# Performance work log

Hardware: AMD Instinct MI355X
Metric: run time of the kernel (lower is better)

## Reference

```python
import jax, jax.numpy as jnp
import numpy as np

B, S, H = 4, 1024, 1024
NH, HD = 16, 64  # num heads, head dim


def setup_inputs() -> dict:
    key = jax.random.key(0)
    ks = jax.random.split(key, 7)
    scale = 1.0 / np.sqrt(H)
    return {
        "hidden_states": jax.random.normal(ks[0], (B, S, H), jnp.float32),
        "attention_mask": jnp.zeros((B, 1, 1, S), jnp.float32),
        "Wq": jax.random.normal(ks[1], (H, H), jnp.float32) * scale,
        "bq": jnp.zeros((H,), jnp.float32),
        "Wk": jax.random.normal(ks[2], (H, H), jnp.float32) * scale,
        "bk": jnp.zeros((H,), jnp.float32),
        "Wv": jax.random.normal(ks[3], (H, H), jnp.float32) * scale,
        "bv": jnp.zeros((H,), jnp.float32),
    }


def _heads(x):
    # [B,S,H] -> [B,NH,S,HD]
    return x.reshape(x.shape[0], x.shape[1], NH, HD).transpose(0, 2, 1, 3)


def reference(hidden_states, attention_mask, Wq, bq, Wk, bk, Wv, bv):
    q = _heads(hidden_states @ Wq + bq)  # [B,NH,S,HD]
    k = _heads(hidden_states @ Wk + bk)
    v = _heads(hidden_states @ Wv + bv)
    scores = jnp.einsum("bhqd,bhkd->bhqk", q, k) / np.sqrt(HD)
    scores = scores + attention_mask  # broadcast additive mask
    probs = jax.nn.softmax(scores, axis=-1)  # dropout p=0 (eval)
    ctx = jnp.einsum("bhqk,bhkd->bhqd", probs, v)
    # [B,NH,S,HD] -> [B,S,H]
    return ctx.transpose(0, 2, 1, 3).reshape(hidden_states.shape[0], hidden_states.shape[1], NH * HD)
```

## Files before the change

kernel.cpp:

```cpp
#include <hip/hip_runtime.h>
#include <hip/hip_bf16.h>

typedef __bf16 bf16_t;
typedef __bf16 bf16x8 __attribute__((ext_vector_type(8)));
typedef float f32x4 __attribute__((ext_vector_type(4)));
typedef float f32x8 __attribute__((ext_vector_type(8)));
typedef float f32x16 __attribute__((ext_vector_type(16)));
typedef unsigned uint2v __attribute__((ext_vector_type(2)));

#define MFMA16(a, b, c) __builtin_amdgcn_mfma_f32_16x16x32_bf16((a), (b), (c), 0, 0, 0)
#define MFMA32(a, b, c) __builtin_amdgcn_mfma_f32_32x32x16_bf16((a), (b), (c), 0, 0, 0)

static constexpr int BB = 4, SS = 1024, HH = 1024, NHEAD = 16, HDIM = 64;
static constexpr int MM = BB * SS;

__device__ __forceinline__ void gload_lds16(const void* g, void* l) {
  __builtin_amdgcn_global_load_lds((const __attribute__((address_space(1))) void*)g,
                                   (__attribute__((address_space(3))) void*)l, 16, 0, 0);
}

#if __has_builtin(__builtin_amdgcn_permlane32_swap)
#define PSWAP(a, b)                                                    \
  {                                                                    \
    uint2v _r = __builtin_amdgcn_permlane32_swap((a), (b), false, false); \
    (a) = _r.x;                                                        \
    (b) = _r.y;                                                        \
  }
#else
#define PSWAP(a, b) asm("v_permlane32_swap_b32 %0, %1" : "+v"(a), "+v"(b))
#endif

__device__ __forceinline__ float EXP2(float x) {
  float r;
  asm("v_exp_f32 %0, %1" : "=v"(r) : "v"(x));
  return r;
}

__global__ __launch_bounds__(256) void prep_kernel(const float* __restrict__ hs,
                                                   const float* __restrict__ Wq,
                                                   const float* __restrict__ Wk,
                                                   const float* __restrict__ Wv,
                                                   bf16_t* __restrict__ hiddenB,
                                                   bf16_t* __restrict__ WT) {
  const int t = threadIdx.x;
  if (blockIdx.x < 2048) {
    int i = (blockIdx.x * 256 + t) * 8;
    float4 a = *(const float4*)(hs + i);
    float4 b = *(const float4*)(hs + i + 4);
    union { int4 i4; bf16_t h[8]; } u;
    u.h[0] = (bf16_t)a.x; u.h[1] = (bf16_t)a.y; u.h[2] = (bf16_t)a.z; u.h[3] = (bf16_t)a.w;
    u.h[4] = (bf16_t)b.x; u.h[5] = (bf16_t)b.y; u.h[6] = (bf16_t)b.z; u.h[7] = (bf16_t)b.w;
    *(int4*)(hiddenB + i) = u.i4;
  } else {
    __shared__ float tile[32][33];
    int id = blockIdx.x - 2048;
    int z = id >> 10;
    int rem = id & 1023;
    int bx = rem & 31, by = rem >> 5;
    const float* W = (z == 0) ? Wq : (z == 1) ? Wk : Wv;
    bf16_t* Out = WT + (size_t)z * HH * HH;
    int tx = t & 31, ty = t >> 5;
    int x0 = bx * 32;
    int y0 = by * 32;
    for (int j = ty; j < 32; j += 8)
      tile[j][tx] = W[(size_t)(y0 + j) * HH + x0 + tx];
    __syncthreads();
    for (int j = ty; j < 32; j += 8)
      Out[(size_t)(x0 + j) * HH + y0 + tx] = (bf16_t)tile[tx][j];
  }
}

#define BMT 128
#define BNT 384
#define BKT 64
#define NTL 16
#define BUFBYTES 65536

__global__ __launch_bounds__(512, 2) void qkv_gemm2(const bf16_t* __restrict__ hiddenB,
                                                    const bf16_t* __restrict__ WT,
                                                    const float* __restrict__ bq,
                                                    const float* __restrict__ bk,
                                                    const float* __restrict__ bv,
                                                    bf16_t* __restrict__ Qo,
                                                    bf16_t* __restrict__ Ko,
                                                    bf16_t* __restrict__ Vt) {
  __shared__ bf16_t smem[2 * BUFBYTES / 2];

  const int wg = blockIdx.x;
  const int id = (wg & 7) * 32 + (wg >> 3);
  const int nb = id & 7;
  const int mb = id >> 3;

  const int t = threadIdx.x;
  const int lane = t & 63;
  const int w = t >> 6;
  const int wr = w >> 2;
  const int wc = w & 3;
  const int lr = lane & 15;
  const int g4 = lane >> 4;

  const unsigned schunk = (((unsigned)(t & 7)) ^ ((unsigned)((t >> 3) & 7))) << 4;
  const char* Ag = (const char*)hiddenB + (size_t)(mb * BMT) * 2048;
  const char* Bg = (const char*)WT + (size_t)(nb * BNT) * 2048;

  auto stage = [&](const char* gb, int growbase, int kbyte, char* ldsdest) {
    gload_lds16(gb + (size_t)(growbase + (t >> 3)) * 2048 + kbyte + schunk,
                ldsdest + w * 1024);
  };
  const unsigned axor = ((unsigned)(lr & 7)) << 4;

  f32x4 acc[4][6] = {};

  {
    char* S0 = (char*)smem;
    stage(Ag, 0, 0, S0);
    stage(Ag, 64, 0, S0 + 8192);
#pragma unroll
    for (int i = 0; i < 6; ++i) stage(Bg, i * 64, 0, S0 + 16384 + i * 8192);
  }
  asm volatile("s_waitcnt vmcnt(0)" ::: "memory");
  __builtin_amdgcn_s_barrier();

  for (int j = 0; j < NTL; ++j) {
    const char* Ab = (const char*)smem + (j & 1) * BUFBYTES;
    const char* Bb = Ab + 16384;
    char* Sb = (char*)smem + ((j + 1) & 1) * BUFBYTES;
    const int kb = (j + 1) * 128;
    const bool st = (j + 1 < NTL);

    if (st) { stage(Ag, 0, kb, Sb); stage(Ag, 64, kb, Sb + 8192); }

    bf16x8 af[4][2];
#pragma unroll
    for (int mi = 0; mi < 4; ++mi)
#pragma unroll
      for (int ks = 0; ks < 2; ++ks)
        af[mi][ks] = *(const bf16x8*)(Ab + (size_t)(wr * 64 + mi * 16 + lr) * 128 +
                                      (((unsigned)(ks * 64 + g4 * 16)) ^ axor));

#pragma unroll
    for (int p = 0; p < 3; ++p) {
      if (st) {
        stage(Bg, (2 * p) * 64, kb, Sb + 16384 + (2 * p) * 8192);
        stage(Bg, (2 * p + 1) * 64, kb, Sb + 16384 + (2 * p + 1) * 8192);
      }
      bf16x8 b0[2], b1[2];
#pragma unroll
      for (int ks = 0; ks < 2; ++ks) {
        b0[ks] = *(const bf16x8*)(Bb + (size_t)(wc * 96 + (2 * p) * 16 + lr) * 128 +
                                  (((unsigned)(ks * 64 + g4 * 16)) ^ axor));
        b1[ks] = *(const bf16x8*)(Bb + (size_t)(wc * 96 + (2 * p + 1) * 16 + lr) * 128 +
                                  (((unsigned)(ks * 64 + g4 * 16)) ^ axor));
      }
      __builtin_amdgcn_s_setprio(1);
#pragma unroll
      for (int mi = 0; mi < 4; ++mi)
#pragma unroll
        for (int ks = 0; ks < 2; ++ks) {
          acc[mi][2 * p] = MFMA16(af[mi][ks], b0[ks], acc[mi][2 * p]);
          acc[mi][2 * p + 1] = MFMA16(af[mi][ks], b1[ks], acc[mi][2 * p + 1]);
        }
      __builtin_amdgcn_s_setprio(0);
    }

    if (st) {
      asm volatile("s_waitcnt vmcnt(0)" ::: "memory");
      __builtin_amdgcn_s_barrier();
    }
  }

#pragma unroll
  for (int ni = 0; ni < 6; ++ni) {
    int col = nb * BNT + wc * 96 + ni * 16 + lr;
    int z = col >> 10;
    int ci = col & 1023;
    const float* bias = (z == 0) ? bq : (z == 1) ? bk : bv;
    float bia = bias[ci];
    int hh = ci >> 6, d = ci & 63;
    if (z < 2) {
      bf16_t* Out = (z == 0) ? Qo : Ko;
#pragma unroll
      for (int mi = 0; mi < 4; ++mi) {
#pragma unroll
        for (int r = 0; r < 4; ++r) {
          int row = mb * BMT + wr * 64 + mi * 16 + g4 * 4 + r;
          int b = row >> 10, s = row & 1023;
          Out[((size_t)(b * NHEAD + hh) * SS + s) * HDIM + d] = (bf16_t)(acc[mi][ni][r] + bia);
        }
      }
    } else {
#pragma unroll
      for (int mi = 0; mi < 4; ++mi) {
        int row0 = mb * BMT + wr * 64 + mi * 16 + g4 * 4;
        int b = row0 >> 10, s0 = row0 & 1023;
        float v0 = acc[mi][ni][0] + bia, v1 = acc[mi][ni][1] + bia;
        float v2 = acc[mi][ni][2] + bia, v3 = acc[mi][ni][3] + bia;
        unsigned u0, u1;
        asm("v_cvt_pk_bf16_f32 %0, %1, %2" : "=v"(u0) : "v"(v0), "v"(v1));
        asm("v_cvt_pk_bf16_f32 %0, %1, %2" : "=v"(u1) : "v"(v2), "v"(v3));
        uint2 pv; pv.x = u0; pv.y = u1;
        *(uint2*)&Vt[((size_t)(b * NHEAD + hh) * HDIM + d) * SS + s0] = pv;
      }
    }
  }
}

__global__ __launch_bounds__(512, 4) void attn8_kernel(const bf16_t* __restrict__ Q,
                                                       const bf16_t* __restrict__ K,
                                                       const bf16_t* __restrict__ Vt,
                                                       const float* __restrict__ mask,
                                                       float* __restrict__ out) {
  __shared__ bf16_t KVsm[2][2][2][64 * 64];
  __shared__ float Msm[SS];

  const int wg = blockIdx.x;
  const int id = (wg & 7) * 64 + (wg >> 3);
  const int xblk = id & 7;
  const int bh = id >> 3;

  const int b = bh >> 4;
  const int h = bh & 15;
  const int t = threadIdx.x;
  const int lane = t & 63;
  const int w = t >> 6;
  const int wl = w & 3;
  const int half = w >> 2;
  const int l31 = lane & 31;
  const int hi = lane >> 5;
  const int q0 = xblk * 128 + wl * 32;
  const int kvbase = half * 512;

  const bf16_t* Qh = Q + (size_t)bh * SS * HDIM;
  const bf16_t* Kh = K + (size_t)bh * SS * HDIM;
  const bf16_t* Vh = Vt + (size_t)bh * HDIM * SS;

  const float L2E = 1.4426950408889634f;
  if (t < 256) {
    float4 mv = *(const float4*)&mask[(size_t)b * SS + t * 4];
    mv.x = mv.x * L2E - 16.f; mv.y = mv.y * L2E - 16.f;
    mv.z = mv.z * L2E - 16.f; mv.w = mv.w * L2E - 16.f;
    *(float4*)&Msm[t * 4] = mv;
  }

  bf16x8 qb[4];
#pragma unroll
  for (int c = 0; c < 4; ++c) {
    bf16x8 q = *(const bf16x8*)&Qh[(size_t)(q0 + l31) * HDIM + c * 16 + hi * 8];
#pragma unroll
    for (int e = 0; e < 8; ++e) q[e] = (bf16_t)((float)q[e] * (0.125f * L2E));
    qb[c] = q;
  }

  const int srow = lane >> 3;
  const unsigned gcol = ((lane & 7) * 16) ^ (srow << 4);
  const unsigned swz = (unsigned)((l31 & 7) << 4);

  auto stageKV = [&](int tile, int buf) {
    const int kv0 = kvbase + tile * 64;
#pragma unroll
    for (int i = 0; i < 2; ++i) {
      int rbase = wl * 16 + i * 8;
      gload_lds16((const char*)Kh + (size_t)(kv0 + rbase + srow) * 128 + gcol,
                  (char*)&KVsm[half][buf][0][0] + (size_t)rbase * 128);
      gload_lds16((const char*)Vh + (size_t)(rbase + srow) * 2048 + (size_t)kv0 * 2 + gcol,
                  (char*)&KVsm[half][buf][1][0] + (size_t)rbase * 128);
    }
  };

  f32x16 acc0 = {}, acc1 = {};
  f32x8 la = {}, lb = {};

  stageKV(0, 0);
  asm volatile("s_waitcnt vmcnt(0) lgkmcnt(0)" ::: "memory");
  __builtin_amdgcn_s_barrier();

  for (int tt = 0; tt < 8; ++tt) {
    if (tt + 1 < 8) stageKV(tt + 1, (tt + 1) & 1);
    const char* Kb = (const char*)&KVsm[half][tt & 1][0][0];
    const char* Vb = (const char*)&KVsm[half][tt & 1][1][0];
    const int kv0 = kvbase + tt * 64;

    f32x16 st0 = {}, st1 = {};
    __builtin_amdgcn_s_setprio(1);
#pragma unroll
    for (int c = 0; c < 4; ++c) {
      bf16x8 kf0 = *(const bf16x8*)(Kb + (size_t)l31 * 128 + ((unsigned)(c * 32 + hi * 16) ^ swz));
      st0 = MFMA32(kf0, qb[c], st0);
    }
#pragma unroll
    for (int c = 0; c < 4; ++c) {
      bf16x8 kf1 = *(const bf16x8*)(Kb + (size_t)(32 + l31) * 128 + ((unsigned)(c * 32 + hi * 16) ^ swz));
      st1 = MFMA32(kf1, qb[c], st1);
    }
    __builtin_amdgcn_s_setprio(0);

#pragma unroll
    for (int k2 = 0; k2 < 8; ++k2) {
      int off = 8 * (k2 >> 1) + 4 * hi + 2 * (k2 & 1);
      float2 m0v = *(const float2*)&Msm[kv0 + off];
      float2 m1v = *(const float2*)&Msm[kv0 + 32 + off];
      st0[2 * k2] += m0v.x; st0[2 * k2 + 1] += m0v.y;
      st1[2 * k2] += m1v.x; st1[2 * k2 + 1] += m1v.y;
    }
#pragma unroll
    for (int r = 0; r < 16; ++r) st0[r] = EXP2(st0[r]);
#pragma unroll
    for (int r = 0; r < 16; ++r) st1[r] = EXP2(st1[r]);

#pragma unroll
    for (int r = 0; r < 8; ++r) {
      la[r] += st0[r] + st0[r + 8];
      lb[r] += st1[r] + st1[r + 8];
    }

    unsigned wd0[8], wd1[8];
#pragma unroll
    for (int k2 = 0; k2 < 8; ++k2) {
      unsigned r0, r1;
      float a0f = st0[2 * k2], a1f = st0[2 * k2 + 1];
      float b0f = st1[2 * k2], b1f = st1[2 * k2 + 1];
      asm("v_cvt_pk_bf16_f32 %0, %1, %2" : "=v"(r0) : "v"(a0f), "v"(a1f));
      asm("v_cvt_pk_bf16_f32 %0, %1, %2" : "=v"(r1) : "v"(b0f), "v"(b1f));
      wd0[k2] = r0; wd1[k2] = r1;
    }
    unsigned a0 = wd0[0], b0 = wd0[2]; PSWAP(a0, b0);
    unsigned a1 = wd0[1], b1 = wd0[3]; PSWAP(a1, b1);
    unsigned a2 = wd0[4], b2 = wd0[6]; PSWAP(a2, b2);
    unsigned a3 = wd0[5], b3 = wd0[7]; PSWAP(a3, b3);
    unsigned c0 = wd1[0], d0 = wd1[2]; PSWAP(c0, d0);
    unsigned c1 = wd1[1], d1 = wd1[3]; PSWAP(c1, d1);
    unsigned c2 = wd1[4], d2 = wd1[6]; PSWAP(c2, d2);
    unsigned c3 = wd1[5], d3 = wd1[7]; PSWAP(c3, d3);
    union { unsigned u[4]; bf16x8 v; } pf0, pf1, pf2, pf3;
    pf0.u[0] = a0; pf0.u[1] = a1; pf0.u[2] = b0; pf0.u[3] = b1;
    pf1.u[0] = a2; pf1.u[1] = a3; pf1.u[2] = b2; pf1.u[3] = b3;
    pf2.u[0] = c0; pf2.u[1] = c1; pf2.u[2] = d0; pf2.u[3] = d1;
    pf3.u[0] = c2; pf3.u[1] = c3; pf3.u[2] = d2; pf3.u[3] = d3;

    __builtin_amdgcn_s_setprio(1);
    {
      bf16x8 vf;
      vf = *(const bf16x8*)(Vb + (size_t)(l31) * 128 + ((unsigned)(0 * 32 + hi * 16) ^ swz));
      acc0 = MFMA32(vf, pf0.v, acc0);
      vf = *(const bf16x8*)(Vb + (size_t)(32 + l31) * 128 + ((unsigned)(0 * 32 + hi * 16) ^ swz));
      acc1 = MFMA32(vf, pf0.v, acc1);
      vf = *(const bf16x8*)(Vb + (size_t)(l31) * 128 + ((unsigned)(1 * 32 + hi * 16) ^ swz));
      acc0 = MFMA32(vf, pf1.v, acc0);
      vf = *(const bf16x8*)(Vb + (size_t)(32 + l31) * 128 + ((unsigned)(1 * 32 + hi * 16) ^ swz));
      acc1 = MFMA32(vf, pf1.v, acc1);
      vf = *(const bf16x8*)(Vb + (size_t)(l31) * 128 + ((unsigned)(2 * 32 + hi * 16) ^ swz));
      acc0 = MFMA32(vf, pf2.v, acc0);
      vf = *(const bf16x8*)(Vb + (size_t)(32 + l31) * 128 + ((unsigned)(2 * 32 + hi * 16) ^ swz));
      acc1 = MFMA32(vf, pf2.v, acc1);
      vf = *(const bf16x8*)(Vb + (size_t)(l31) * 128 + ((unsigned)(3 * 32 + hi * 16) ^ swz));
      acc0 = MFMA32(vf, pf3.v, acc0);
      vf = *(const bf16x8*)(Vb + (size_t)(32 + l31) * 128 + ((unsigned)(3 * 32 + hi * 16) ^ swz));
      acc1 = MFMA32(vf, pf3.v, acc1);
    }
    __builtin_amdgcn_s_setprio(0);

    asm volatile("s_waitcnt vmcnt(0)" ::: "memory");
    __builtin_amdgcn_s_barrier();
  }

  float l_run;
  {
    float s0 = (la[0] + lb[0]) + (la[1] + lb[1]);
    float s1 = (la[2] + lb[2]) + (la[3] + lb[3]);
    float s2 = (la[4] + lb[4]) + (la[5] + lb[5]);
    float s3 = (la[6] + lb[6]) + (la[7] + lb[7]);
    l_run = (s0 + s1) + (s2 + s3);
    l_run += __shfl_xor(l_run, 32);
  }

  __syncthreads();
  float* mb = (float*)&KVsm[0][0][0][0];
  if (half == 1) {
    float* dst = mb + ((size_t)(wl * 64 + lane)) * 36;
#pragma unroll
    for (int g = 0; g < 4; ++g) {
      float4 w0, w1;
      w0.x = acc0[g * 4 + 0]; w0.y = acc0[g * 4 + 1];
      w0.z = acc0[g * 4 + 2]; w0.w = acc0[g * 4 + 3];
      w1.x = acc1[g * 4 + 0]; w1.y = acc1[g * 4 + 1];
      w1.z = acc1[g * 4 + 2]; w1.w = acc1[g * 4 + 3];
      *(float4*)(dst + g * 4) = w0;
      *(float4*)(dst + 16 + g * 4) = w1;
    }
    dst[32] = l_run;
  }
  __syncthreads();
  if (half == 0) {
    const float* src = mb + ((size_t)(wl * 64 + lane)) * 36;
    float rinv = 1.0f / (l_run + src[32]);
    int q = q0 + l31;
    float* ob = out + ((size_t)(b * SS + q)) * HH + h * HDIM;
#pragma unroll
    for (int g = 0; g < 4; ++g) {
      float4 o0, o1;
      o0.x = (acc0[g * 4 + 0] + src[g * 4 + 0]) * rinv;
      o0.y = (acc0[g * 4 + 1] + src[g * 4 + 1]) * rinv;
      o0.z = (acc0[g * 4 + 2] + src[g * 4 + 2]) * rinv;
      o0.w = (acc0[g * 4 + 3] + src[g * 4 + 3]) * rinv;
      o1.x = (acc1[g * 4 + 0] + src[16 + g * 4 + 0]) * rinv;
      o1.y = (acc1[g * 4 + 1] + src[16 + g * 4 + 1]) * rinv;
      o1.z = (acc1[g * 4 + 2] + src[16 + g * 4 + 2]) * rinv;
      o1.w = (acc1[g * 4 + 3] + src[16 + g * 4 + 3]) * rinv;
      *(float4*)&ob[g * 8 + 4 * hi] = o0;
      *(float4*)&ob[32 + g * 8 + 4 * hi] = o1;
    }
  }
}

extern "C" void kernel_launch(void* const* d_in, const int* in_sizes, int n_in,
                              void* d_out, int out_size, void* d_ws, size_t ws_size,
                              hipStream_t stream) {
  const float* hs   = (const float*)d_in[0];
  const float* mask = (const float*)d_in[1];
  const float* Wq   = (const float*)d_in[2];
  const float* bq   = (const float*)d_in[3];
  const float* Wk   = (const float*)d_in[4];
  const float* bk   = (const float*)d_in[5];
  const float* Wv   = (const float*)d_in[6];
  const float* bv   = (const float*)d_in[7];
  float* out = (float*)d_out;

  char* ws = (char*)d_ws;
  bf16_t* hiddenB = (bf16_t*)ws;
  bf16_t* WT      = (bf16_t*)(ws + (size_t)8 * 1024 * 1024);
  bf16_t* Qb      = (bf16_t*)(ws + (size_t)14 * 1024 * 1024);
  bf16_t* Kb      = (bf16_t*)(ws + (size_t)22 * 1024 * 1024);
  bf16_t* Vt      = (bf16_t*)(ws + (size_t)30 * 1024 * 1024);

  prep_kernel<<<2048 + 3072, 256, 0, stream>>>(hs, Wq, Wk, Wv, hiddenB, WT);
  qkv_gemm2<<<256, 512, 0, stream>>>(hiddenB, WT, bq, bk, bv, Qb, Kb, Vt);
  attn8_kernel<<<512, 512, 0, stream>>>(Qb, Kb, Vt, mask, out);
}
```

Measured before the change: 72.60 us.

## Deepen QKV GEMM prefetch to two tiles ahead with register-staged fragments

The QKV projection GEMM now keeps two K-tiles in flight. It loads all A and B fragments for the current tile into registers, then barriers and reuses that same LDS buffer to prefetch tile j+2 before running the MFMAs. A partial vmcnt wait lets the next tile's loads land while the newer ones are still outstanding. The aim is to hide global-to-LDS latency better than single-step double buffering. In exchange it raises register pressure (all B fragments held at once) and adds an extra barrier per iteration.

```diff
diff --git a/kernel.cpp b/kernel.cpp
--- a/kernel.cpp
+++ b/kernel.cpp
@@ -76,7 +76,7 @@
 #define NTL 16
 #define BUFBYTES 65536
 
-__global__ __launch_bounds__(512, 2) void qkv_gemm2(const bf16_t* __restrict__ hiddenB,
+__global__ __launch_bounds__(512, 2) void qkv_gemm3(const bf16_t* __restrict__ hiddenB,
                                                     const bf16_t* __restrict__ WT,
                                                     const float* __restrict__ bq,
                                                     const float* __restrict__ bk,
@@ -107,64 +107,61 @@
     gload_lds16(gb + (size_t)(growbase + (t >> 3)) * 2048 + kbyte + schunk,
                 ldsdest + w * 1024);
   };
+  auto stage_tile = [&](int kt, char* Sb) {
+    const int kb = kt * 128;
+    stage(Ag, 0, kb, Sb);
+    stage(Ag, 64, kb, Sb + 8192);
+#pragma unroll
+    for (int i = 0; i < 6; ++i) stage(Bg, i * 64, kb, Sb + 16384 + i * 8192);
+  };
   const unsigned axor = ((unsigned)(lr & 7)) << 4;
 
   f32x4 acc[4][6] = {};
 
-  {
-    char* S0 = (char*)smem;
-    stage(Ag, 0, 0, S0);
-    stage(Ag, 64, 0, S0 + 8192);
-#pragma unroll
-    for (int i = 0; i < 6; ++i) stage(Bg, i * 64, 0, S0 + 16384 + i * 8192);
-  }
-  asm volatile("s_waitcnt vmcnt(0)" ::: "memory");
+  stage_tile(0, (char*)smem);
+  stage_tile(1, (char*)smem + BUFBYTES);
+  asm volatile("s_waitcnt vmcnt(8)" ::: "memory");
   __builtin_amdgcn_s_barrier();
 
   for (int j = 0; j < NTL; ++j) {
     const char* Ab = (const char*)smem + (j & 1) * BUFBYTES;
     const char* Bb = Ab + 16384;
-    char* Sb = (char*)smem + ((j + 1) & 1) * BUFBYTES;
-    const int kb = (j + 1) * 128;
-    const bool st = (j + 1 < NTL);
-
-    if (st) { stage(Ag, 0, kb, Sb); stage(Ag, 64, kb, Sb + 8192); }
-
-    bf16x8 af[4][2];
+
+    bf16x8 af[4][2], bfr[6][2];
 #pragma unroll
     for (int mi = 0; mi < 4; ++mi)
 #pragma unroll
       for (int ks = 0; ks < 2; ++ks)
         af[mi][ks] = *(const bf16x8*)(Ab + (size_t)(wr * 64 + mi * 16 + lr) * 128 +
                                       (((unsigned)(ks * 64 + g4 * 16)) ^ axor));
-
-#pragma unroll
-    for (int p = 0; p < 3; ++p) {
-      if (st) {
-        stage(Bg, (2 * p) * 64, kb, Sb + 16384 + (2 * p) * 8192);
-        stage(Bg, (2 * p + 1) * 64, kb, Sb + 16384 + (2 * p + 1) * 8192);
-      }
-      bf16x8 b0[2], b1[2];
-#pragma unroll
-      for (int ks = 0; ks < 2; ++ks) {
-        b0[ks] = *(const bf16x8*)(Bb + (size_t)(wc * 96 + (2 * p) * 16 + lr) * 128 +
-                                  (((unsigned)(ks * 64 + g4 * 16)) ^ axor));
-        b1[ks] = *(const bf16x8*)(Bb + (size_t)(wc * 96 + (2 * p + 1) * 16 + lr) * 128 +
-                                  (((unsigned)(ks * 64 + g4 * 16)) ^ axor));
-      }
-      __builtin_amdgcn_s_setprio(1);
-#pragma unroll
-      for (int mi = 0; mi < 4; ++mi)
-#pragma unroll
-        for (int ks = 0; ks < 2; ++ks) {
-          acc[mi][2 * p] = MFMA16(af[mi][ks], b0[ks], acc[mi][2 * p]);
-          acc[mi][2 * p + 1] = MFMA16(af[mi][ks], b1[ks], acc[mi][2 * p + 1]);
-        }
-      __builtin_amdgcn_s_setprio(0);
-    }
-
-    if (st) {
-      asm volatile("s_waitcnt vmcnt(0)" ::: "memory");
+#pragma unroll
+    for (int ni = 0; ni < 6; ++ni)
+#pragma unroll
+      for (int ks = 0; ks < 2; ++ks)
+        bfr[ni][ks] = *(const bf16x8*)(Bb + (size_t)(wc * 96 + ni * 16 + lr) * 128 +
+                                       (((unsigned)(ks * 64 + g4 * 16)) ^ axor));
+
+    asm volatile("s_waitcnt lgkmcnt(0)" ::: "memory");
+    __builtin_amdgcn_sched_barrier(0);
+    __builtin_amdgcn_s_barrier();
+
+    if (j + 2 < NTL) stage_tile(j + 2, (char*)smem + (j & 1) * BUFBYTES);
+
+    __builtin_amdgcn_s_setprio(1);
+#pragma unroll
+    for (int mi = 0; mi < 4; ++mi)
+#pragma unroll
+      for (int ni = 0; ni < 6; ++ni)
+#pragma unroll
+        for (int ks = 0; ks < 2; ++ks)
+          acc[mi][ni] = MFMA16(af[mi][ks], bfr[ni][ks], acc[mi][ni]);
+    __builtin_amdgcn_s_setprio(0);
+
+    if (j + 1 < NTL) {
+      if (j + 2 < NTL)
+        asm volatile("s_waitcnt vmcnt(8)" ::: "memory");
+      else
+        asm volatile("s_waitcnt vmcnt(0)" ::: "memory");
       __builtin_amdgcn_s_barrier();
     }
   }
@@ -433,6 +430,6 @@
   bf16_t* Vt      = (bf16_t*)(ws + (size_t)30 * 1024 * 1024);
 
   prep_kernel<<<2048 + 3072, 256, 0, stream>>>(hs, Wq, Wk, Wv, hiddenB, WT);
-  qkv_gemm2<<<256, 512, 0, stream>>>(hiddenB, WT, bq, bk, bv, Qb, Kb, Vt);
+  qkv_gemm3<<<256, 512, 0, stream>>>(hiddenB, WT, bq, bk, bv, Qb, Kb, Vt);
   attn8_kernel<<<512, 512, 0, stream>>>(Qb, Kb, Vt, mask, out);
 }
```

Result: no change. 74.04 us (+2.0%).
